# Kernel tuning notes

Measured on AMD Instinct MI355X. Metric: run time of the kernel, lower is better.

## Reference

```python
import jax, jax.numpy as jnp
import numpy as np

NEG_INF = -1e9  # large negative for masking (avoid NaN rows under -inf with fully masked rows)
LEAKY_SLOPE = 0.2

def setup_inputs() -> dict:
    key = jax.random.key(0)
    k1, k2, k3, k4, k5 = jax.random.split(key, 5)
    N, in_dim, out_dim = 8192, 512, 64
    x = jax.random.normal(k1, (N, in_dim), dtype=jnp.float32)
    adj = jax.random.randint(k2, (N, N), 0, 2, dtype=jnp.int32)
    W = jax.random.normal(k3, (out_dim, in_dim), dtype=jnp.float32) * (1.0 / np.sqrt(in_dim))
    a_src = jax.random.normal(k4, (out_dim,), dtype=jnp.float32)
    a_dst = jax.random.normal(k5, (out_dim,), dtype=jnp.float32)
    return {"x": x, "adj": adj, "W": W, "a_src": a_src, "a_dst": a_dst}

def reference(x, adj, W, a_src, a_dst):
    # Linear projection: Wh[n, d]
    Wh = x @ W.T
    # Additive GAT attention: e[i, j] = LeakyReLU(a_src . Wh_i + a_dst . Wh_j)
    s = Wh @ a_src  # [N]
    d = Wh @ a_dst  # [N]
    e = jax.nn.leaky_relu(s[:, None] + d[None, :], negative_slope=LEAKY_SLOPE)  # [N, N]
    e = jnp.where(adj > 0, e, NEG_INF)
    alpha = jax.nn.softmax(e, axis=1)  # [N, N]
    # Dropout on alpha is identity in eval/reference mode.
    h_prime = alpha @ Wh  # [N, out_dim]
    return h_prime
```

## Files before the change

### kernel.cpp

```cpp
#include <hip/hip_runtime.h>
#include <hip/hip_bf16.h>

#define GN 8192
#define IN_DIM 512
#define ODIM 64
#define SLOPE 0.2f
#define JSPLIT 16
#define JCH (GN / JSPLIT)
#define LSTRIDE 68
#define NTILE 4

typedef __attribute__((ext_vector_type(4))) float  f32x4;
typedef __attribute__((ext_vector_type(4))) int    i32x4;
typedef __attribute__((ext_vector_type(8))) short  bf16x8;
typedef __attribute__((ext_vector_type(4))) unsigned short u16x4;

static __device__ __forceinline__ float bf2f(unsigned short u) {
    return __uint_as_float(((unsigned)u) << 16);
}
static __device__ __forceinline__ unsigned short f2bf(float f) {
    union { float f; unsigned u; } c; c.f = f;
    unsigned b = c.u;
    return (unsigned short)((b + 0x7fffu + ((b >> 16) & 1u)) >> 16);
}

static __device__ __forceinline__ bf16x8 load8(const void* p, size_t off, int f32) {
    if (f32) {
        f32x4 lo = *(const f32x4*)((const float*)p + off);
        f32x4 hi = *(const f32x4*)((const float*)p + off + 4);
        bf16x8 r;
        #pragma unroll
        for (int q = 0; q < 4; ++q) {
            r[q]     = (short)f2bf(lo[q]);
            r[4 + q] = (short)f2bf(hi[q]);
        }
        return r;
    }
    return *(const bf16x8*)((const ushort*)p + off);
}

extern "C" __global__ __launch_bounds__(256)
void gat_proj(const void* __restrict__ x_, const void* __restrict__ W_,
              const void* __restrict__ as_, const void* __restrict__ ad_,
              ushort* __restrict__ WhTp, float* __restrict__ s_arr,
              float* __restrict__ d_arr, int* __restrict__ dmax_bits,
              int* __restrict__ dflag, float* __restrict__ accum,
              float* __restrict__ lsum)
{
    {
        f32x4 z = {0.f, 0.f, 0.f, 0.f};
        f32x4* ap = (f32x4*)(accum + (size_t)blockIdx.x * 4096);
        #pragma unroll
        for (int k = 0; k < 4; ++k) ap[k * 256 + threadIdx.x] = z;
        if (threadIdx.x < 64) lsum[blockIdx.x * 64 + threadIdx.x] = 0.f;
    }
    const int wave = threadIdx.x >> 6;
    const int lane = threadIdx.x & 63;
    unsigned xw = ((const unsigned*)x_)[lane];
    unsigned ef = (xw >> 23) & 0xffu;
    unsigned long long vt = __ballot(ef > 60u && ef < 180u);
    const int f32 = (__popcll(vt) >= 32) ? 1 : 0;
    if (blockIdx.x == 0 && threadIdx.x == 0) *dflag = f32;

    const int quad = lane >> 4;
    const int lq   = lane & 15;
    const int i0   = blockIdx.x * 64 + wave * 16;

    f32x4 acc[4] = {{0,0,0,0},{0,0,0,0},{0,0,0,0},{0,0,0,0}};
    const size_t arow = (size_t)(i0 + lq) * IN_DIM;
    #pragma unroll 2
    for (int k0 = 0; k0 < IN_DIM; k0 += 32) {
        const int kk = k0 + quad * 8;
        bf16x8 a  = load8(x_, arow + kk, f32);
        bf16x8 b0 = load8(W_, (size_t)( 0 + lq) * IN_DIM + kk, f32);
        bf16x8 b1 = load8(W_, (size_t)(16 + lq) * IN_DIM + kk, f32);
        bf16x8 b2 = load8(W_, (size_t)(32 + lq) * IN_DIM + kk, f32);
        bf16x8 b3 = load8(W_, (size_t)(48 + lq) * IN_DIM + kk, f32);
        acc[0] = __builtin_amdgcn_mfma_f32_16x16x32_bf16(a, b0, acc[0], 0, 0, 0);
        acc[1] = __builtin_amdgcn_mfma_f32_16x16x32_bf16(a, b1, acc[1], 0, 0, 0);
        acc[2] = __builtin_amdgcn_mfma_f32_16x16x32_bf16(a, b2, acc[2], 0, 0, 0);
        acc[3] = __builtin_amdgcn_mfma_f32_16x16x32_bf16(a, b3, acc[3], 0, 0, 0);
    }
    float av_s[4], av_d[4];
    #pragma unroll
    for (int t = 0; t < 4; ++t) {
        const int n = t * 16 + lq;
        av_s[t] = f32 ? ((const float*)as_)[n] : bf2f(((const ushort*)as_)[n]);
        av_d[t] = f32 ? ((const float*)ad_)[n] : bf2f(((const ushort*)ad_)[n]);
    }
    #pragma unroll
    for (int t = 0; t < 4; ++t) {
        u16x4 pk;
        #pragma unroll
        for (int r = 0; r < 4; ++r) pk[r] = f2bf(acc[t][r]);
        const size_t hw = ((size_t)((i0 >> 3) + (quad >> 1)) * 64 + t * 16 + lq) * 8
                          + (quad & 1) * 4;
        *(u16x4*)(WhTp + hw) = pk;
    }
    float ps[4], pd[4];
    #pragma unroll
    for (int r = 0; r < 4; ++r) {
        float s = 0.f, d = 0.f;
        #pragma unroll
        for (int t = 0; t < 4; ++t) {
            s = fmaf(acc[t][r], av_s[t], s);
            d = fmaf(acc[t][r], av_d[t], d);
        }
        #pragma unroll
        for (int off = 1; off < 16; off <<= 1) {
            s += __shfl_xor(s, off);
            d += __shfl_xor(d, off);
        }
        ps[r] = s; pd[r] = d;
    }
    if (lq == 0) {
        float dmx = -1e30f;
        #pragma unroll
        for (int r = 0; r < 4; ++r) {
            s_arr[i0 + quad * 4 + r] = ps[r];
            d_arr[i0 + quad * 4 + r] = pd[r];
            dmx = fmaxf(dmx, pd[r]);
        }
        if (dmx > 0.f) atomicMax(dmax_bits, __float_as_int(dmx));
    }
}

extern "C" __global__ __launch_bounds__(256)
void gat_attn(const int* __restrict__ adj, const ushort* __restrict__ WhTp,
              const float* __restrict__ s_arr, const float* __restrict__ d_arr,
              const int* __restrict__ dmax_bits,
              float* __restrict__ accum, float* __restrict__ lsum)
{
    __shared__ unsigned char mb[2][64 * LSTRIDE];
    const int b    = blockIdx.x;
    const int ib   = 127 - (b & 127);
    const int js0  = b >> 7;
    const int wave = threadIdx.x >> 6;
    const int lane = threadIdx.x & 63;
    const int quad = lane >> 4;
    const int lq   = lane & 15;
    const int i0   = ib * 64;
    const int li   = wave * 16 + lq;
    const int i    = i0 + li;
    const float dmax = __int_as_float(*dmax_bits);
    const float si = s_arr[i];
    const float tbv = si + dmax;
    const float mi = fmaxf(tbv, SLOPE * tbv);
    const float k1 = si - mi;
    const float k2 = SLOPE * si - mi;

    const size_t adjbase = (size_t)i0 * GN + lane * 8;

    i32x4 ra[6], rb[6];
    auto issue = [&](int c, int jb) {
        const int* rp = adj + adjbase + (size_t)(c * 4 + wave) * GN + jb;
        ra[c % 6] = ((const i32x4*)rp)[0];
        rb[c % 6] = ((const i32x4*)rp)[1];
    };
    auto pack = [&](int c, int bufsel) {
        const i32x4 va = ra[c % 6], vb = rb[c % 6];
        unsigned byte = 0;
        #pragma unroll
        for (int q = 0; q < 4; ++q) {
            byte |= (va[q] > 0 ? 1u : 0u) << q;
            byte |= (vb[q] > 0 ? 1u : 0u) << (4 + q);
        }
        mb[bufsel][(c * 4 + wave) * LSTRIDE + lane] = (unsigned char)byte;
    };

    f32x4 acc0 = {0,0,0,0}, acc1 = {0,0,0,0}, acc2 = {0,0,0,0}, acc3 = {0,0,0,0};
    f32x4 acc4 = {0,0,0,0};
    bf16x8 ones;
    #pragma unroll
    for (int q = 0; q < 8; ++q) ones[q] = (short)0x3F80;

    const int jb0 = (js0 + 4 * (NTILE - 1)) * JCH;

    #pragma unroll
    for (int c = 0; c < 16; ++c) {
        issue(c, jb0);
        if (c >= 5) pack(c - 5, 0);
    }
    pack(11, 0); pack(12, 0); pack(13, 0); pack(14, 0); pack(15, 0);
    __syncthreads();

    f32x4 dv0 = *(const f32x4*)(d_arr + jb0 + quad * 8);
    f32x4 dv1 = *(const f32x4*)(d_arr + jb0 + quad * 8 + 4);
    const ushort* bb0 = WhTp + ((size_t)(jb0 >> 3) + quad) * 512;
    bf16x8 b0 = *(const bf16x8*)(bb0 + ( 0 + lq) * 8);
    bf16x8 b1 = *(const bf16x8*)(bb0 + (16 + lq) * 8);
    bf16x8 b2 = *(const bf16x8*)(bb0 + (32 + lq) * 8);
    bf16x8 b3 = *(const bf16x8*)(bb0 + (48 + lq) * 8);

    #pragma unroll 1
    for (int t = 0; t < NTILE; ++t) {
        const int jb   = (js0 + 4 * (NTILE - 1 - t)) * JCH;
        const int jbn  = jb - 4 * JCH;
        const bool more = (t < NTILE - 1);
        const int buf  = t & 1, nbuf = buf ^ 1;

        #pragma unroll
        for (int it = 0; it < 16; ++it) {
            const int jtb = (it < 15) ? jb : (more ? jbn : jb);
            const int itn = (it < 15) ? (it + 1) : 0;
            const int jn  = jtb + itn * 32 + quad * 8;
            f32x4 ndv0 = *(const f32x4*)(d_arr + jn);
            f32x4 ndv1 = *(const f32x4*)(d_arr + jn + 4);
            const ushort* nb = WhTp + ((size_t)(jtb >> 3) + itn * 4 + quad) * 512;
            bf16x8 nb0 = *(const bf16x8*)(nb + ( 0 + lq) * 8);
            bf16x8 nb1 = *(const bf16x8*)(nb + (16 + lq) * 8);
            bf16x8 nb2 = *(const bf16x8*)(nb + (32 + lq) * 8);
            bf16x8 nb3 = *(const bf16x8*)(nb + (48 + lq) * 8);
            if (more) issue(it, jbn);
            if (more && it >= 5) pack(it - 5, nbuf);
            unsigned bw = *(const unsigned*)(&mb[buf][li * LSTRIDE + it * 4]);
            const unsigned m8 = (bw >> (quad * 8)) & 0xffu;
            float w[8];
            #pragma unroll
            for (int q = 0; q < 4; ++q) {
                float a0 = fmaxf(dv0[q] + k1, fmaf(SLOPE, dv0[q], k2));
                float v0 = __expf(a0);
                w[q] = ((m8 >> q) & 1u) ? v0 : 0.f;
                float a1 = fmaxf(dv1[q] + k1, fmaf(SLOPE, dv1[q], k2));
                float v1 = __expf(a1);
                w[4 + q] = ((m8 >> (4 + q)) & 1u) ? v1 : 0.f;
            }
            union { bf16x8 v; __hip_bfloat162 h[4]; } af;
            #pragma unroll
            for (int q = 0; q < 4; ++q)
                af.h[q] = __float22bfloat162_rn(make_float2(w[2 * q], w[2 * q + 1]));
            acc0 = __builtin_amdgcn_mfma_f32_16x16x32_bf16(af.v, b0, acc0, 0, 0, 0);
            acc1 = __builtin_amdgcn_mfma_f32_16x16x32_bf16(af.v, b1, acc1, 0, 0, 0);
            acc2 = __builtin_amdgcn_mfma_f32_16x16x32_bf16(af.v, b2, acc2, 0, 0, 0);
            acc3 = __builtin_amdgcn_mfma_f32_16x16x32_bf16(af.v, b3, acc3, 0, 0, 0);
            acc4 = __builtin_amdgcn_mfma_f32_16x16x32_bf16(af.v, ones, acc4, 0, 0, 0);
            dv0 = ndv0; dv1 = ndv1; b0 = nb0; b1 = nb1; b2 = nb2; b3 = nb3;
        }
        if (more) {
            pack(11, nbuf); pack(12, nbuf); pack(13, nbuf);
            pack(14, nbuf); pack(15, nbuf);
        }
        __syncthreads();
    }

    const int orow = i0 + wave * 16 + quad * 4;
    if (lq == 0) {
        #pragma unroll
        for (int r = 0; r < 4; ++r) atomicAdd(&lsum[orow + r], acc4[r]);
    }
    #pragma unroll
    for (int r = 0; r < 4; ++r) {
        atomicAdd(&accum[(size_t)(orow + r) * ODIM +  0 + lq], acc0[r]);
        atomicAdd(&accum[(size_t)(orow + r) * ODIM + 16 + lq], acc1[r]);
        atomicAdd(&accum[(size_t)(orow + r) * ODIM + 32 + lq], acc2[r]);
        atomicAdd(&accum[(size_t)(orow + r) * ODIM + 48 + lq], acc3[r]);
    }
}

extern "C" __global__ __launch_bounds__(256)
void gat_final(const float* __restrict__ accum, const float* __restrict__ lsum,
               const int* __restrict__ flag, void* __restrict__ out)
{
    const int idx = blockIdx.x * 256 + threadIdx.x;
    const float v = accum[idx] / lsum[idx >> 6];
    if (*flag) ((float*)out)[idx] = v;
    else       ((ushort*)out)[idx] = f2bf(v);
}

extern "C" void kernel_launch(void* const* d_in, const int* in_sizes, int n_in,
                              void* d_out, int out_size, void* d_ws, size_t ws_size,
                              hipStream_t stream)
{
    const void* x     = d_in[0];
    const int*  adj   = (const int*)d_in[1];
    const void* W     = d_in[2];
    const void* a_src = d_in[3];
    const void* a_dst = d_in[4];

    char* ws = (char*)d_ws;
    size_t off = 0;
    int* dmax_bits = (int*)(ws + off);  off += 128;
    int* dflag = (int*)(ws + off);      off += 128;
    size_t zero_bytes = off;
    float* accum = (float*)(ws + off);  off += (size_t)GN * ODIM * 4;
    float* lsum  = (float*)(ws + off);  off += (size_t)GN * 4;
    float* s_arr = (float*)(ws + off);  off += (size_t)GN * 4;
    float* d_arr = (float*)(ws + off);  off += (size_t)GN * 4;
    ushort* WhTp = (ushort*)(ws + off); off += (size_t)ODIM * GN * 2;

    hipMemsetAsync(ws, 0, zero_bytes, stream);
    gat_proj<<<GN / 64, 256, 0, stream>>>(x, W, a_src, a_dst,
                                          WhTp, s_arr, d_arr, dmax_bits, dflag,
                                          accum, lsum);
    gat_attn<<<512, 256, 0, stream>>>(adj, WhTp, s_arr, d_arr,
                                      dmax_bits, accum, lsum);
    gat_final<<<GN * ODIM / 256, 256, 0, stream>>>(accum, lsum, dflag, d_out);
}
```

Baseline: 426.8 us.

## Factor exp of LeakyReLU into precomputed per-column exponentials and load adj directly

Precomputes exp(d_j) and exp(0.2*d_j) per column in the projection kernel, so each attention weight becomes max(A_i*E1_j, B_i*E2_j) instead of a per-element exp. It also drops the LDS bitmask staging and barriers, and has each lane read its own adjacency row segment directly into registers with a 4-deep prefetch. This removes the exp work and the shared-memory synchronisation. In exchange the adj reads are less coalesced, and the product form risks overflow or underflow (E1 is clamped at 87) and a slight loss of precision.

Measured after the change: 447.3 us. 4.8% more time.

```diff
diff --git a/kernel.cpp b/kernel.cpp
--- a/kernel.cpp
+++ b/kernel.cpp
@@ -7,7 +7,6 @@
 #define SLOPE 0.2f
 #define JSPLIT 16
 #define JCH (GN / JSPLIT)
-#define LSTRIDE 68
 #define NTILE 4
 
 typedef __attribute__((ext_vector_type(4))) float  f32x4;
@@ -43,9 +42,9 @@
 void gat_proj(const void* __restrict__ x_, const void* __restrict__ W_,
               const void* __restrict__ as_, const void* __restrict__ ad_,
               ushort* __restrict__ WhTp, float* __restrict__ s_arr,
-              float* __restrict__ d_arr, int* __restrict__ dmax_bits,
-              int* __restrict__ dflag, float* __restrict__ accum,
-              float* __restrict__ lsum)
+              float* __restrict__ E1, float* __restrict__ E2,
+              int* __restrict__ dmax_bits, int* __restrict__ dflag,
+              float* __restrict__ accum, float* __restrict__ lsum)
 {
     {
         f32x4 z = {0.f, 0.f, 0.f, 0.f};
@@ -117,9 +116,12 @@
         float dmx = -1e30f;
         #pragma unroll
         for (int r = 0; r < 4; ++r) {
-            s_arr[i0 + quad * 4 + r] = ps[r];
-            d_arr[i0 + quad * 4 + r] = pd[r];
-            dmx = fmaxf(dmx, pd[r]);
+            const int n = i0 + quad * 4 + r;
+            const float dv = pd[r];
+            s_arr[n] = ps[r];
+            E1[n] = __expf(fminf(dv, 87.f));
+            E2[n] = __expf(SLOPE * dv);
+            dmx = fmaxf(dmx, dv);
         }
         if (dmx > 0.f) atomicMax(dmax_bits, __float_as_int(dmx));
     }
@@ -127,11 +129,11 @@
 
 extern "C" __global__ __launch_bounds__(256)
 void gat_attn(const int* __restrict__ adj, const ushort* __restrict__ WhTp,
-              const float* __restrict__ s_arr, const float* __restrict__ d_arr,
+              const float* __restrict__ s_arr,
+              const float* __restrict__ E1, const float* __restrict__ E2,
               const int* __restrict__ dmax_bits,
               float* __restrict__ accum, float* __restrict__ lsum)
 {
-    __shared__ unsigned char mb[2][64 * LSTRIDE];
     const int b    = blockIdx.x;
     const int ib   = 127 - (b & 127);
     const int js0  = b >> 7;
@@ -140,33 +142,20 @@
     const int quad = lane >> 4;
     const int lq   = lane & 15;
     const int i0   = ib * 64;
-    const int li   = wave * 16 + lq;
-    const int i    = i0 + li;
+    const int i    = i0 + wave * 16 + lq;
+
     const float dmax = __int_as_float(*dmax_bits);
-    const float si = s_arr[i];
+    const float si  = s_arr[i];
     const float tbv = si + dmax;
-    const float mi = fmaxf(tbv, SLOPE * tbv);
-    const float k1 = si - mi;
-    const float k2 = SLOPE * si - mi;
-
-    const size_t adjbase = (size_t)i0 * GN + lane * 8;
-
-    i32x4 ra[6], rb[6];
-    auto issue = [&](int c, int jb) {
-        const int* rp = adj + adjbase + (size_t)(c * 4 + wave) * GN + jb;
-        ra[c % 6] = ((const i32x4*)rp)[0];
-        rb[c % 6] = ((const i32x4*)rp)[1];
-    };
-    auto pack = [&](int c, int bufsel) {
-        const i32x4 va = ra[c % 6], vb = rb[c % 6];
-        unsigned byte = 0;
-        #pragma unroll
-        for (int q = 0; q < 4; ++q) {
-            byte |= (va[q] > 0 ? 1u : 0u) << q;
-            byte |= (vb[q] > 0 ? 1u : 0u) << (4 + q);
-        }
-        mb[bufsel][(c * 4 + wave) * LSTRIDE + lane] = (unsigned char)byte;
-    };
+    const float mi  = fmaxf(tbv, SLOPE * tbv);
+    const float Aw  = __expf(si - mi);
+    const float Bw  = __expf(SLOPE * si - mi);
+
+    const size_t rowbase = (size_t)i * GN + quad * 8;
+
+    #define COLOF(u) ((js0 + 4 * (NTILE - 1 - ((u) >> 4))) * JCH + ((u) & 15) * 32)
+
+    i32x4 ra[4], rb[4];
 
     f32x4 acc0 = {0,0,0,0}, acc1 = {0,0,0,0}, acc2 = {0,0,0,0}, acc3 = {0,0,0,0};
     f32x4 acc4 = {0,0,0,0};
@@ -174,56 +163,56 @@
     #pragma unroll
     for (int q = 0; q < 8; ++q) ones[q] = (short)0x3F80;
 
-    const int jb0 = (js0 + 4 * (NTILE - 1)) * JCH;
-
-    #pragma unroll
-    for (int c = 0; c < 16; ++c) {
-        issue(c, jb0);
-        if (c >= 5) pack(c - 5, 0);
-    }
-    pack(11, 0); pack(12, 0); pack(13, 0); pack(14, 0); pack(15, 0);
-    __syncthreads();
-
-    f32x4 dv0 = *(const f32x4*)(d_arr + jb0 + quad * 8);
-    f32x4 dv1 = *(const f32x4*)(d_arr + jb0 + quad * 8 + 4);
-    const ushort* bb0 = WhTp + ((size_t)(jb0 >> 3) + quad) * 512;
-    bf16x8 b0 = *(const bf16x8*)(bb0 + ( 0 + lq) * 8);
-    bf16x8 b1 = *(const bf16x8*)(bb0 + (16 + lq) * 8);
-    bf16x8 b2 = *(const bf16x8*)(bb0 + (32 + lq) * 8);
-    bf16x8 b3 = *(const bf16x8*)(bb0 + (48 + lq) * 8);
+    #pragma unroll
+    for (int c = 0; c < 4; ++c) {
+        const int* p = adj + rowbase + COLOF(c);
+        ra[c] = ((const i32x4*)p)[0];
+        rb[c] = ((const i32x4*)p)[1];
+    }
+    f32x4 e1a, e1b, e2a, e2b;
+    bf16x8 b0, b1, b2, b3;
+    {
+        const int col = COLOF(0);
+        const float* p1 = E1 + col + quad * 8;
+        const float* p2 = E2 + col + quad * 8;
+        e1a = *(const f32x4*)p1; e1b = *(const f32x4*)(p1 + 4);
+        e2a = *(const f32x4*)p2; e2b = *(const f32x4*)(p2 + 4);
+        const ushort* nb = WhTp + ((size_t)(col >> 3) + quad) * 512;
+        b0 = *(const bf16x8*)(nb + ( 0 + lq) * 8);
+        b1 = *(const bf16x8*)(nb + (16 + lq) * 8);
+        b2 = *(const bf16x8*)(nb + (32 + lq) * 8);
+        b3 = *(const bf16x8*)(nb + (48 + lq) * 8);
+    }
 
     #pragma unroll 1
     for (int t = 0; t < NTILE; ++t) {
-        const int jb   = (js0 + 4 * (NTILE - 1 - t)) * JCH;
-        const int jbn  = jb - 4 * JCH;
-        const bool more = (t < NTILE - 1);
-        const int buf  = t & 1, nbuf = buf ^ 1;
-
         #pragma unroll
         for (int it = 0; it < 16; ++it) {
-            const int jtb = (it < 15) ? jb : (more ? jbn : jb);
-            const int itn = (it < 15) ? (it + 1) : 0;
-            const int jn  = jtb + itn * 32 + quad * 8;
-            f32x4 ndv0 = *(const f32x4*)(d_arr + jn);
-            f32x4 ndv1 = *(const f32x4*)(d_arr + jn + 4);
-            const ushort* nb = WhTp + ((size_t)(jtb >> 3) + itn * 4 + quad) * 512;
+            const int u = t * 16 + it;
+            const i32x4 va = ra[it & 3], vb = rb[it & 3];
+            if (t < NTILE - 1 || it < 12) {
+                const int* p = adj + rowbase + COLOF(u + 4);
+                ra[it & 3] = ((const i32x4*)p)[0];
+                rb[it & 3] = ((const i32x4*)p)[1];
+            }
+            const int un  = (u < NTILE * 16 - 1) ? u + 1 : u;
+            const int ncol = COLOF(un);
+            const float* p1 = E1 + ncol + quad * 8;
+            const float* p2 = E2 + ncol + quad * 8;
+            f32x4 ne1a = *(const f32x4*)p1, ne1b = *(const f32x4*)(p1 + 4);
+            f32x4 ne2a = *(const f32x4*)p2, ne2b = *(const f32x4*)(p2 + 4);
+            const ushort* nb = WhTp + ((size_t)(ncol >> 3) + quad) * 512;
             bf16x8 nb0 = *(const bf16x8*)(nb + ( 0 + lq) * 8);
             bf16x8 nb1 = *(const bf16x8*)(nb + (16 + lq) * 8);
             bf16x8 nb2 = *(const bf16x8*)(nb + (32 + lq) * 8);
             bf16x8 nb3 = *(const bf16x8*)(nb + (48 + lq) * 8);
-            if (more) issue(it, jbn);
-            if (more && it >= 5) pack(it - 5, nbuf);
-            unsigned bw = *(const unsigned*)(&mb[buf][li * LSTRIDE + it * 4]);
-            const unsigned m8 = (bw >> (quad * 8)) & 0xffu;
             float w[8];
             #pragma unroll
             for (int q = 0; q < 4; ++q) {
-                float a0 = fmaxf(dv0[q] + k1, fmaf(SLOPE, dv0[q], k2));
-                float v0 = __expf(a0);
-                w[q] = ((m8 >> q) & 1u) ? v0 : 0.f;
-                float a1 = fmaxf(dv1[q] + k1, fmaf(SLOPE, dv1[q], k2));
-                float v1 = __expf(a1);
-                w[4 + q] = ((m8 >> (4 + q)) & 1u) ? v1 : 0.f;
+                const float w0 = fmaxf(Aw * e1a[q], Bw * e2a[q]);
+                const float w1 = fmaxf(Aw * e1b[q], Bw * e2b[q]);
+                w[q]     = (va[q] > 0) ? w0 : 0.f;
+                w[4 + q] = (vb[q] > 0) ? w1 : 0.f;
             }
             union { bf16x8 v; __hip_bfloat162 h[4]; } af;
             #pragma unroll
@@ -234,14 +223,11 @@
             acc2 = __builtin_amdgcn_mfma_f32_16x16x32_bf16(af.v, b2, acc2, 0, 0, 0);
             acc3 = __builtin_amdgcn_mfma_f32_16x16x32_bf16(af.v, b3, acc3, 0, 0, 0);
             acc4 = __builtin_amdgcn_mfma_f32_16x16x32_bf16(af.v, ones, acc4, 0, 0, 0);
-            dv0 = ndv0; dv1 = ndv1; b0 = nb0; b1 = nb1; b2 = nb2; b3 = nb3;
-        }
-        if (more) {
-            pack(11, nbuf); pack(12, nbuf); pack(13, nbuf);
-            pack(14, nbuf); pack(15, nbuf);
-        }
-        __syncthreads();
-    }
+            e1a = ne1a; e1b = ne1b; e2a = ne2a; e2b = ne2b;
+            b0 = nb0; b1 = nb1; b2 = nb2; b3 = nb3;
+        }
+    }
+    #undef COLOF
 
     const int orow = i0 + wave * 16 + quad * 4;
     if (lq == 0) {
@@ -285,14 +271,15 @@
     float* accum = (float*)(ws + off);  off += (size_t)GN * ODIM * 4;
     float* lsum  = (float*)(ws + off);  off += (size_t)GN * 4;
     float* s_arr = (float*)(ws + off);  off += (size_t)GN * 4;
-    float* d_arr = (float*)(ws + off);  off += (size_t)GN * 4;
+    float* E1    = (float*)(ws + off);  off += (size_t)GN * 4;
+    float* E2    = (float*)(ws + off);  off += (size_t)GN * 4;
     ushort* WhTp = (ushort*)(ws + off); off += (size_t)ODIM * GN * 2;
 
     hipMemsetAsync(ws, 0, zero_bytes, stream);
     gat_proj<<<GN / 64, 256, 0, stream>>>(x, W, a_src, a_dst,
-                                          WhTp, s_arr, d_arr, dmax_bits, dflag,
+                                          WhTp, s_arr, E1, E2, dmax_bits, dflag,
                                           accum, lsum);
-    gat_attn<<<512, 256, 0, stream>>>(adj, WhTp, s_arr, d_arr,
+    gat_attn<<<512, 256, 0, stream>>>(adj, WhTp, s_arr, E1, E2,
                                       dmax_bits, accum, lsum);
     gat_final<<<GN * ODIM / 256, 256, 0, stream>>>(accum, lsum, dflag, d_out);
 }
```

## Factor attention exponentials into per-row and per-column terms staged in LDS

Applied to the files above, without the earlier changes.

Uses exp(max(a,b)) = max(exp(a),exp(b)) to split each attention weight into a product of a per-row factor and a precomputed per-column factor (exp(d) and exp(0.2*d)). The projection kernel now computes these column exponentials once, and the attention kernel stages its column slice in shared memory, replacing per-element expf with two multiplies and a max. The aim is to cut transcendental work in the inner loop. In exchange it uses more shared memory and risks overflow or underflow in the factored products, since column values are clamped only at 87.

Measured after the change: 423.9 us. About the same (-0.7%).

```diff
diff --git a/kernel.cpp b/kernel.cpp
--- a/kernel.cpp
+++ b/kernel.cpp
@@ -39,13 +39,17 @@
     return *(const bf16x8*)((const ushort*)p + off);
 }
 
+static __device__ __forceinline__ int colof(int js0, int u) {
+    return (js0 + 4 * (NTILE - 1 - (u >> 4))) * JCH + (u & 15) * 32;
+}
+
 extern "C" __global__ __launch_bounds__(256)
 void gat_proj(const void* __restrict__ x_, const void* __restrict__ W_,
               const void* __restrict__ as_, const void* __restrict__ ad_,
               ushort* __restrict__ WhTp, float* __restrict__ s_arr,
-              float* __restrict__ d_arr, int* __restrict__ dmax_bits,
-              int* __restrict__ dflag, float* __restrict__ accum,
-              float* __restrict__ lsum)
+              float* __restrict__ E1, float* __restrict__ E2,
+              int* __restrict__ dmax_bits, int* __restrict__ dflag,
+              float* __restrict__ accum, float* __restrict__ lsum)
 {
     {
         f32x4 z = {0.f, 0.f, 0.f, 0.f};
@@ -117,9 +121,12 @@
         float dmx = -1e30f;
         #pragma unroll
         for (int r = 0; r < 4; ++r) {
-            s_arr[i0 + quad * 4 + r] = ps[r];
-            d_arr[i0 + quad * 4 + r] = pd[r];
-            dmx = fmaxf(dmx, pd[r]);
+            const int n = i0 + quad * 4 + r;
+            const float dv = pd[r];
+            s_arr[n] = ps[r];
+            E1[n] = __expf(fminf(dv, 87.f));
+            E2[n] = __expf(SLOPE * dv);
+            dmx = fmaxf(dmx, dv);
         }
         if (dmx > 0.f) atomicMax(dmax_bits, __float_as_int(dmx));
     }
@@ -127,11 +134,13 @@
 
 extern "C" __global__ __launch_bounds__(256)
 void gat_attn(const int* __restrict__ adj, const ushort* __restrict__ WhTp,
-              const float* __restrict__ s_arr, const float* __restrict__ d_arr,
+              const float* __restrict__ s_arr,
+              const float* __restrict__ E1, const float* __restrict__ E2,
               const int* __restrict__ dmax_bits,
               float* __restrict__ accum, float* __restrict__ lsum)
 {
     __shared__ unsigned char mb[2][64 * LSTRIDE];
+    __shared__ float lE[2 * NTILE * 512];
     const int b    = blockIdx.x;
     const int ib   = 127 - (b & 127);
     const int js0  = b >> 7;
@@ -146,8 +155,17 @@
     const float si = s_arr[i];
     const float tbv = si + dmax;
     const float mi = fmaxf(tbv, SLOPE * tbv);
-    const float k1 = si - mi;
-    const float k2 = SLOPE * si - mi;
+    const float Aw = __expf(si - mi);
+    const float Bw = __expf(SLOPE * si - mi);
+
+    {
+        const int m0 = threadIdx.x * 8;
+        const int gcol = colof(js0, m0 >> 5) + (m0 & 31);
+        *(f32x4*)&lE[m0]            = *(const f32x4*)(E1 + gcol);
+        *(f32x4*)&lE[m0 + 4]        = *(const f32x4*)(E1 + gcol + 4);
+        *(f32x4*)&lE[2048 + m0]     = *(const f32x4*)(E2 + gcol);
+        *(f32x4*)&lE[2048 + m0 + 4] = *(const f32x4*)(E2 + gcol + 4);
+    }
 
     const size_t adjbase = (size_t)i0 * GN + lane * 8;
 
@@ -184,8 +202,6 @@
     pack(11, 0); pack(12, 0); pack(13, 0); pack(14, 0); pack(15, 0);
     __syncthreads();
 
-    f32x4 dv0 = *(const f32x4*)(d_arr + jb0 + quad * 8);
-    f32x4 dv1 = *(const f32x4*)(d_arr + jb0 + quad * 8 + 4);
     const ushort* bb0 = WhTp + ((size_t)(jb0 >> 3) + quad) * 512;
     bf16x8 b0 = *(const bf16x8*)(bb0 + ( 0 + lq) * 8);
     bf16x8 b1 = *(const bf16x8*)(bb0 + (16 + lq) * 8);
@@ -201,11 +217,9 @@
 
         #pragma unroll
         for (int it = 0; it < 16; ++it) {
+            const int u = t * 16 + it;
             const int jtb = (it < 15) ? jb : (more ? jbn : jb);
             const int itn = (it < 15) ? (it + 1) : 0;
-            const int jn  = jtb + itn * 32 + quad * 8;
-            f32x4 ndv0 = *(const f32x4*)(d_arr + jn);
-            f32x4 ndv1 = *(const f32x4*)(d_arr + jn + 4);
             const ushort* nb = WhTp + ((size_t)(jtb >> 3) + itn * 4 + quad) * 512;
             bf16x8 nb0 = *(const bf16x8*)(nb + ( 0 + lq) * 8);
             bf16x8 nb1 = *(const bf16x8*)(nb + (16 + lq) * 8);
@@ -215,15 +229,18 @@
             if (more && it >= 5) pack(it - 5, nbuf);
             unsigned bw = *(const unsigned*)(&mb[buf][li * LSTRIDE + it * 4]);
             const unsigned m8 = (bw >> (quad * 8)) & 0xffu;
+            const float* pe = lE + u * 32 + quad * 8;
+            const f32x4 e1a = *(const f32x4*)pe;
+            const f32x4 e1b = *(const f32x4*)(pe + 4);
+            const f32x4 e2a = *(const f32x4*)(pe + 2048);
+            const f32x4 e2b = *(const f32x4*)(pe + 2052);
             float w[8];
             #pragma unroll
             for (int q = 0; q < 4; ++q) {
-                float a0 = fmaxf(dv0[q] + k1, fmaf(SLOPE, dv0[q], k2));
-                float v0 = __expf(a0);
-                w[q] = ((m8 >> q) & 1u) ? v0 : 0.f;
-                float a1 = fmaxf(dv1[q] + k1, fmaf(SLOPE, dv1[q], k2));
-                float v1 = __expf(a1);
-                w[4 + q] = ((m8 >> (4 + q)) & 1u) ? v1 : 0.f;
+                const float w0 = fmaxf(Aw * e1a[q], Bw * e2a[q]);
+                const float w1 = fmaxf(Aw * e1b[q], Bw * e2b[q]);
+                w[q]     = (m8 & (1u << q))       ? w0 : 0.f;
+                w[4 + q] = (m8 & (1u << (4 + q))) ? w1 : 0.f;
             }
             union { bf16x8 v; __hip_bfloat162 h[4]; } af;
             #pragma unroll
@@ -234,7 +251,7 @@
             acc2 = __builtin_amdgcn_mfma_f32_16x16x32_bf16(af.v, b2, acc2, 0, 0, 0);
             acc3 = __builtin_amdgcn_mfma_f32_16x16x32_bf16(af.v, b3, acc3, 0, 0, 0);
             acc4 = __builtin_amdgcn_mfma_f32_16x16x32_bf16(af.v, ones, acc4, 0, 0, 0);
-            dv0 = ndv0; dv1 = ndv1; b0 = nb0; b1 = nb1; b2 = nb2; b3 = nb3;
+            b0 = nb0; b1 = nb1; b2 = nb2; b3 = nb3;
         }
         if (more) {
             pack(11, nbuf); pack(12, nbuf); pack(13, nbuf);
@@ -285,14 +302,15 @@
     float* accum = (float*)(ws + off);  off += (size_t)GN * ODIM * 4;
     float* lsum  = (float*)(ws + off);  off += (size_t)GN * 4;
     float* s_arr = (float*)(ws + off);  off += (size_t)GN * 4;
-    float* d_arr = (float*)(ws + off);  off += (size_t)GN * 4;
+    float* E1    = (float*)(ws + off);  off += (size_t)GN * 4;
+    float* E2    = (float*)(ws + off);  off += (size_t)GN * 4;
     ushort* WhTp = (ushort*)(ws + off); off += (size_t)ODIM * GN * 2;
 
     hipMemsetAsync(ws, 0, zero_bytes, stream);
     gat_proj<<<GN / 64, 256, 0, stream>>>(x, W, a_src, a_dst,
-                                          WhTp, s_arr, d_arr, dmax_bits, dflag,
+                                          WhTp, s_arr, E1, E2, dmax_bits, dflag,
                                           accum, lsum);
-    gat_attn<<<512, 256, 0, stream>>>(adj, WhTp, s_arr, d_arr,
+    gat_attn<<<512, 256, 0, stream>>>(adj, WhTp, s_arr, E1, E2,
                                       dmax_bits, accum, lsum);
     gat_final<<<GN * ODIM / 256, 256, 0, stream>>>(accum, lsum, dflag, d_out);
 }
```
